# Kernel optimization log

Measured on AMD Instinct MI355X. Metric: run time of the kernel, lower is better.

## Reference

```python
import jax, jax.numpy as jnp
import numpy as np

TAU = 0.5  # init tau
EPS = 1e-8  # F.cosine_similarity eps


def setup_inputs() -> dict:
    key = jax.random.key(0)
    k1, k2 = jax.random.split(key)
    N, D, NUM_CLASSES = 4096, 1024, 128
    layer_embeds = jax.random.normal(k1, (N, D), dtype=jnp.float32)
    y_true = jax.random.randint(k2, (N,), 0, NUM_CLASSES, dtype=jnp.int64)
    return {"layer_embeds": layer_embeds, "y_true": y_true}


def reference(layer_embeds, y_true):
    N = layer_embeds.shape[0]
    # batched cosine similarity, scaled like the original: (cos + 1) * 0.5 * tau
    norms = jnp.maximum(jnp.linalg.norm(layer_embeds, axis=1), EPS)  # [N]
    cos = (layer_embeds @ layer_embeds.T) / (norms[:, None] * norms[None, :])  # [N, N]
    S = (cos + 1.0) * 0.5 * TAU

    same = y_true[:, None] == y_true[None, :]  # [N, N]
    eye = jnp.eye(N, dtype=bool)
    pos_mask = same & ~eye            # same-label pairs, j != i
    neg_mask = ~same                  # different-label pairs (diag excluded since same there)

    # column 0: first positive (in j order), else stays 0
    has_pos = pos_mask.any(axis=1)
    first_pos = jnp.argmax(pos_mask, axis=1)
    pos_val = jnp.where(has_pos, S[jnp.arange(N), first_pos], 0.0)  # [N]

    # negatives fill columns 1.. in j order: col = 1 + (#negatives with j' < j)
    negi = neg_mask.astype(jnp.int32)
    col = 1 + jnp.cumsum(negi, axis=1) - negi  # [N, N]
    W = 2 * N  # pad one dummy column for non-negative entries
    cols = jnp.where(neg_mask, col, W - 1)
    rows = jnp.broadcast_to(jnp.arange(N)[:, None], (N, N))
    loss_temp = jnp.zeros((N, W), dtype=jnp.float32)
    loss_temp = loss_temp.at[rows, cols].set(jnp.where(neg_mask, S, 0.0))
    loss_temp = loss_temp.at[:, 0].set(pos_val)
    loss_temp = loss_temp[:, : 2 * N - 1]  # [N, 2N-1], matches torch buffer

    # -log_softmax, take column 0, sum over rows, divide by N
    lse = jax.nn.logsumexp(loss_temp, axis=1)  # [N]
    loss = jnp.sum(lse - loss_temp[:, 0]) / N
    return loss
```

## Files before the change

### kernel.cpp

```cpp
#include <hip/hip_runtime.h>
#include <hip/hip_bf16.h>
#include <math.h>

#define NN 4096
#define DD 1024
#define NCLS 128
#define TAU 0.5f
#define EPSV 1e-8f

typedef __bf16 bf16;
typedef __bf16 bf16x8 __attribute__((ext_vector_type(8)));
typedef __bf16 bf16x4 __attribute__((ext_vector_type(4)));
typedef float f32x4 __attribute__((ext_vector_type(4)));

__device__ __forceinline__ void gl2lds16(const void* g, void* l) {
    __builtin_amdgcn_global_load_lds(
        (const __attribute__((address_space(1))) void*)g,
        (__attribute__((address_space(3))) void*)l,
        16, 0, 0);
}

__global__ __launch_bounds__(256) void k_norm_cast(const float* __restrict__ X,
                                                   bf16* __restrict__ Xn,
                                                   float* __restrict__ rsum) {
    int w = threadIdx.x >> 6, lane = threadIdx.x & 63;
    int row = blockIdx.x * 4 + w;
    const float* xr = X + (size_t)row * DD;
    float4 v[4];
    float ss = 0.f;
#pragma unroll
    for (int c = 0; c < 4; ++c) {
        v[c] = *(const float4*)(xr + c * 256 + lane * 4);
        ss += v[c].x * v[c].x + v[c].y * v[c].y + v[c].z * v[c].z + v[c].w * v[c].w;
    }
#pragma unroll
    for (int m = 1; m < 64; m <<= 1) ss += __shfl_xor(ss, m, 64);
    float rn = 1.f / fmaxf(sqrtf(ss), EPSV);
    if (lane == 0) rsum[row] = 0.f;
#pragma unroll
    for (int c = 0; c < 4; ++c) {
        bf16x4 o;
        o.x = (bf16)(v[c].x * rn);
        o.y = (bf16)(v[c].y * rn);
        o.z = (bf16)(v[c].z * rn);
        o.w = (bf16)(v[c].w * rn);
        *(bf16x4*)(Xn + (size_t)row * DD + c * 256 + lane * 4) = o;
    }
}

__global__ __launch_bounds__(1024) void k_classes(const int* __restrict__ y,
                                                  int* __restrict__ cnt,
                                                  int* __restrict__ mn1,
                                                  int* __restrict__ mn2) {
    __shared__ int sc[NCLS], s1[NCLS], s2[NCLS];
    int t = threadIdx.x;
    if (t < NCLS) { sc[t] = 0; s1[t] = 0x7fffffff; s2[t] = 0x7fffffff; }
    __syncthreads();
    int yv[4];
#pragma unroll
    for (int k = 0; k < 4; ++k) {
        int i = t + k * 1024;
        yv[k] = y[i];
        atomicAdd(&sc[yv[k]], 1);
        atomicMin(&s1[yv[k]], i);
    }
    __syncthreads();
#pragma unroll
    for (int k = 0; k < 4; ++k) {
        int i = t + k * 1024;
        if (s1[yv[k]] != i) atomicMin(&s2[yv[k]], i);
    }
    __syncthreads();
    if (t < NCLS) { cnt[t] = sc[t]; mn1[t] = s1[t]; mn2[t] = s2[t]; }
}

__global__ __launch_bounds__(256) void k_posval(const bf16* __restrict__ Xn,
                                                const int* __restrict__ y,
                                                const int* __restrict__ cnt,
                                                const int* __restrict__ mn1,
                                                const int* __restrict__ mn2,
                                                float* __restrict__ posv) {
    int w = threadIdx.x >> 6, lane = threadIdx.x & 63;
    int i = blockIdx.x * 4 + w;
    int c = y[i];
    float pv = 0.f;
    if (cnt[c] >= 2) {
        int fp = (mn1[c] == i) ? mn2[c] : mn1[c];
        const bf16* xi = Xn + (size_t)i * DD;
        const bf16* xf = Xn + (size_t)fp * DD;
        float dot = 0.f;
#pragma unroll
        for (int cc = 0; cc < 2; ++cc) {
            bf16x8 a = *(const bf16x8*)(xi + cc * 512 + lane * 8);
            bf16x8 b = *(const bf16x8*)(xf + cc * 512 + lane * 8);
#pragma unroll
            for (int e = 0; e < 8; ++e) dot += (float)a[e] * (float)b[e];
        }
#pragma unroll
        for (int m = 1; m < 64; m <<= 1) dot += __shfl_xor(dot, m, 64);
        pv = (dot + 1.f) * (0.5f * TAU);
    }
    if (lane == 0) posv[i] = pv;
}

__global__ __launch_bounds__(256) void k_gemm(const bf16* __restrict__ Xn,
                                              const int* __restrict__ y,
                                              float* __restrict__ rowsum) {
    __shared__ __align__(16) bf16 As[128 * 32];
    __shared__ __align__(16) bf16 Bs[128 * 32];
    __shared__ int yA[128], yB[128];

    int id = blockIdx.x;
    float ff = sqrtf((float)(8 * id + 1));
    int bj = (int)((ff - 1.f) * 0.5f);
    if (bj * (bj + 1) / 2 > id) bj--;
    if ((bj + 1) * (bj + 2) / 2 <= id) bj++;
    int bi = id - bj * (bj + 1) / 2;
    const int rowA0 = bi * 128;
    const int rowB0 = bj * 128;
    const bool diag = (bi == bj);

    const int tid = threadIdx.x;
    if (tid < 128) yA[tid] = y[rowA0 + tid];
    else           yB[tid - 128] = y[rowB0 + tid - 128];

    const int lane = tid & 63;
    const int w = tid >> 6;
    const int wm = w & 1, wn = w >> 1;
    const int lr = lane >> 4, lc = lane & 15;

    f32x4 acc[4][4];
#pragma unroll
    for (int i = 0; i < 4; ++i)
#pragma unroll
        for (int j = 0; j < 4; ++j) acc[i][j] = (f32x4){0.f, 0.f, 0.f, 0.f};

    const int r = tid >> 2;
    const int g = tid & 3;
    const int kg = g ^ ((r >> 1) & 3);
    const bf16* gA0 = Xn + (size_t)(rowA0 + r) * DD + kg * 8;
    const bf16* gA1 = gA0 + (size_t)64 * DD;
    const bf16* gB0 = Xn + (size_t)(rowB0 + r) * DD + kg * 8;
    const bf16* gB1 = gB0 + (size_t)64 * DD;
    bf16* lA0 = As + tid * 8;
    bf16* lA1 = As + 64 * 32 + tid * 8;
    bf16* lB0 = Bs + tid * 8;
    bf16* lB1 = Bs + 64 * 32 + tid * 8;

    const int sw = (lc >> 1) & 3;

    for (int k0 = 0; k0 < DD; k0 += 32) {
        __syncthreads();
        gl2lds16(gA0 + k0, lA0);
        gl2lds16(gA1 + k0, lA1);
        gl2lds16(gB0 + k0, lB0);
        gl2lds16(gB1 + k0, lB1);
        __syncthreads();

        bf16x8 af[4], bfr[4];
#pragma unroll
        for (int mt = 0; mt < 4; ++mt)
            af[mt] = *(const bf16x8*)(As + (wm * 64 + mt * 16 + lc) * 32 + ((lr ^ sw) * 8));
#pragma unroll
        for (int nt = 0; nt < 4; ++nt)
            bfr[nt] = *(const bf16x8*)(Bs + (wn * 64 + nt * 16 + lc) * 32 + ((lr ^ sw) * 8));
#pragma unroll
        for (int mt = 0; mt < 4; ++mt)
#pragma unroll
            for (int nt = 0; nt < 4; ++nt)
                acc[mt][nt] = __builtin_amdgcn_mfma_f32_16x16x32_bf16(
                    af[mt], bfr[nt], acc[mt][nt], 0, 0, 0);
    }

    int ycol[4];
#pragma unroll
    for (int nt = 0; nt < 4; ++nt) ycol[nt] = yB[wn * 64 + nt * 16 + lc];
    float colacc[4] = {0.f, 0.f, 0.f, 0.f};
#pragma unroll
    for (int mt = 0; mt < 4; ++mt) {
#pragma unroll
        for (int rr = 0; rr < 4; ++rr) {
            int rloc = wm * 64 + mt * 16 + lr * 4 + rr;
            int yrow = yA[rloc];
            float s = 0.f;
#pragma unroll
            for (int nt = 0; nt < 4; ++nt) {
                float Sv = (acc[mt][nt][rr] + 1.f) * (0.5f * TAU);
                float e = (ycol[nt] != yrow) ? __expf(Sv) : 0.f;
                s += e;
                colacc[nt] += e;
            }
            s += __shfl_xor(s, 1, 16);
            s += __shfl_xor(s, 2, 16);
            s += __shfl_xor(s, 4, 16);
            s += __shfl_xor(s, 8, 16);
            if (lc == 0) atomicAdd(&rowsum[rowA0 + rloc], s);
        }
    }
    if (!diag) {
#pragma unroll
        for (int nt = 0; nt < 4; ++nt) {
            float cs = colacc[nt];
            cs += __shfl_xor(cs, 16, 64);
            cs += __shfl_xor(cs, 32, 64);
            if (lane < 16) atomicAdd(&rowsum[rowB0 + wn * 64 + nt * 16 + lane], cs);
        }
    }
}

__global__ __launch_bounds__(1024) void k_finalize(const float* __restrict__ rowsum,
                                                   const float* __restrict__ posv,
                                                   const int* __restrict__ y,
                                                   const int* __restrict__ cnt,
                                                   float* __restrict__ out) {
    int t = threadIdx.x;
    float acc = 0.f;
#pragma unroll
    for (int k = 0; k < 4; ++k) {
        int i = t + k * 1024;
        float pv = posv[i];
        float tot = rowsum[i] + __expf(pv) + (float)(NN - 2 + cnt[y[i]]);
        acc += logf(tot) - pv;
    }
#pragma unroll
    for (int m = 1; m < 64; m <<= 1) acc += __shfl_xor(acc, m, 64);
    __shared__ float wsum[16];
    int w = t >> 6, lane = t & 63;
    if (lane == 0) wsum[w] = acc;
    __syncthreads();
    if (t == 0) {
        float s = 0.f;
#pragma unroll
        for (int q = 0; q < 16; ++q) s += wsum[q];
        *out = s / (float)NN;
    }
}

extern "C" void kernel_launch(void* const* d_in, const int* in_sizes, int n_in,
                              void* d_out, int out_size, void* d_ws, size_t ws_size,
                              hipStream_t stream) {
    const float* X = (const float*)d_in[0];
    const int* y = (const int*)d_in[1];
    float* out = (float*)d_out;

    char* ws = (char*)d_ws;
    bf16* Xn     = (bf16*)ws;
    float* rsum  = (float*)(ws + 8 * 1024 * 1024);
    float* posv  = (float*)(ws + 8 * 1024 * 1024 + 16 * 1024);
    int* cnt     = (int*)(ws + 8 * 1024 * 1024 + 32 * 1024);
    int* mn1     = (int*)(ws + 8 * 1024 * 1024 + 32 * 1024 + 512);
    int* mn2     = (int*)(ws + 8 * 1024 * 1024 + 32 * 1024 + 1024);

    k_norm_cast<<<dim3(NN / 4), 256, 0, stream>>>(X, Xn, rsum);
    k_classes<<<dim3(1), 1024, 0, stream>>>(y, cnt, mn1, mn2);
    k_posval<<<dim3(NN / 4), 256, 0, stream>>>(Xn, y, cnt, mn1, mn2, posv);
    k_gemm<<<dim3(528), 256, 0, stream>>>(Xn, y, rsum);
    k_finalize<<<dim3(1), 1024, 0, stream>>>(rsum, posv, y, cnt, out);
}
```

Before: 106.5 us.

## Fuse prep kernels, merge posval into finalize, and deepen GEMM K-tile

Merges class statistics into the normalize/cast kernel (block 0), and folds the positive-value dot product into a parallel finalize kernel that reduces with one atomicAdd per block, going from five launches to three. The GEMM now stages 64-wide K tiles with an 8-way XOR swizzle, halving the number of barrier pairs per K loop. The cost is double the LDS per block and a float atomic reduction whose summation order is nondeterministic.

Result: slower. 127.5 us (+19.7%).

```diff
diff --git a/kernel.cpp b/kernel.cpp
--- a/kernel.cpp
+++ b/kernel.cpp
@@ -20,9 +20,14 @@
         16, 0, 0);
 }
 
-__global__ __launch_bounds__(256) void k_norm_cast(const float* __restrict__ X,
-                                                   bf16* __restrict__ Xn,
-                                                   float* __restrict__ rsum) {
+__global__ __launch_bounds__(256) void k_prep(const float* __restrict__ X,
+                                              bf16* __restrict__ Xn,
+                                              float* __restrict__ rsum,
+                                              const int* __restrict__ y,
+                                              int* __restrict__ cnt,
+                                              int* __restrict__ mn1,
+                                              int* __restrict__ mn2,
+                                              float* __restrict__ out) {
     int w = threadIdx.x >> 6, lane = threadIdx.x & 63;
     int row = blockIdx.x * 4 + w;
     const float* xr = X + (size_t)row * DD;
@@ -46,68 +51,37 @@
         o.w = (bf16)(v[c].w * rn);
         *(bf16x4*)(Xn + (size_t)row * DD + c * 256 + lane * 4) = o;
     }
-}
-
-__global__ __launch_bounds__(1024) void k_classes(const int* __restrict__ y,
-                                                  int* __restrict__ cnt,
-                                                  int* __restrict__ mn1,
-                                                  int* __restrict__ mn2) {
-    __shared__ int sc[NCLS], s1[NCLS], s2[NCLS];
-    int t = threadIdx.x;
-    if (t < NCLS) { sc[t] = 0; s1[t] = 0x7fffffff; s2[t] = 0x7fffffff; }
-    __syncthreads();
-    int yv[4];
-#pragma unroll
-    for (int k = 0; k < 4; ++k) {
-        int i = t + k * 1024;
-        yv[k] = y[i];
-        atomicAdd(&sc[yv[k]], 1);
-        atomicMin(&s1[yv[k]], i);
-    }
-    __syncthreads();
-#pragma unroll
-    for (int k = 0; k < 4; ++k) {
-        int i = t + k * 1024;
-        if (s1[yv[k]] != i) atomicMin(&s2[yv[k]], i);
-    }
-    __syncthreads();
-    if (t < NCLS) { cnt[t] = sc[t]; mn1[t] = s1[t]; mn2[t] = s2[t]; }
-}
-
-__global__ __launch_bounds__(256) void k_posval(const bf16* __restrict__ Xn,
-                                                const int* __restrict__ y,
-                                                const int* __restrict__ cnt,
-                                                const int* __restrict__ mn1,
-                                                const int* __restrict__ mn2,
-                                                float* __restrict__ posv) {
-    int w = threadIdx.x >> 6, lane = threadIdx.x & 63;
-    int i = blockIdx.x * 4 + w;
-    int c = y[i];
-    float pv = 0.f;
-    if (cnt[c] >= 2) {
-        int fp = (mn1[c] == i) ? mn2[c] : mn1[c];
-        const bf16* xi = Xn + (size_t)i * DD;
-        const bf16* xf = Xn + (size_t)fp * DD;
-        float dot = 0.f;
-#pragma unroll
-        for (int cc = 0; cc < 2; ++cc) {
-            bf16x8 a = *(const bf16x8*)(xi + cc * 512 + lane * 8);
-            bf16x8 b = *(const bf16x8*)(xf + cc * 512 + lane * 8);
-#pragma unroll
-            for (int e = 0; e < 8; ++e) dot += (float)a[e] * (float)b[e];
-        }
-#pragma unroll
-        for (int m = 1; m < 64; m <<= 1) dot += __shfl_xor(dot, m, 64);
-        pv = (dot + 1.f) * (0.5f * TAU);
-    }
-    if (lane == 0) posv[i] = pv;
+
+    if (blockIdx.x == 0) {
+        __shared__ int sc[NCLS], s1[NCLS], s2[NCLS];
+        int t = threadIdx.x;
+        if (t < NCLS) { sc[t] = 0; s1[t] = 0x7fffffff; s2[t] = 0x7fffffff; }
+        __syncthreads();
+        int yv[16];
+#pragma unroll
+        for (int k = 0; k < 16; ++k) {
+            int i = k * 256 + t;
+            yv[k] = y[i];
+            atomicAdd(&sc[yv[k]], 1);
+            atomicMin(&s1[yv[k]], i);
+        }
+        __syncthreads();
+#pragma unroll
+        for (int k = 0; k < 16; ++k) {
+            int i = k * 256 + t;
+            if (s1[yv[k]] != i) atomicMin(&s2[yv[k]], i);
+        }
+        __syncthreads();
+        if (t < NCLS) { cnt[t] = sc[t]; mn1[t] = s1[t]; mn2[t] = s2[t]; }
+        if (t == 0) out[0] = 0.f;
+    }
 }
 
 __global__ __launch_bounds__(256) void k_gemm(const bf16* __restrict__ Xn,
                                               const int* __restrict__ y,
                                               float* __restrict__ rowsum) {
-    __shared__ __align__(16) bf16 As[128 * 32];
-    __shared__ __align__(16) bf16 Bs[128 * 32];
+    __shared__ __align__(16) bf16 As[128 * 64];
+    __shared__ __align__(16) bf16 Bs[128 * 64];
     __shared__ int yA[128], yB[128];
 
     int id = blockIdx.x;
@@ -135,41 +109,47 @@
 #pragma unroll
         for (int j = 0; j < 4; ++j) acc[i][j] = (f32x4){0.f, 0.f, 0.f, 0.f};
 
-    const int r = tid >> 2;
-    const int g = tid & 3;
-    const int kg = g ^ ((r >> 1) & 3);
-    const bf16* gA0 = Xn + (size_t)(rowA0 + r) * DD + kg * 8;
-    const bf16* gA1 = gA0 + (size_t)64 * DD;
-    const bf16* gB0 = Xn + (size_t)(rowB0 + r) * DD + kg * 8;
-    const bf16* gB1 = gB0 + (size_t)64 * DD;
-    bf16* lA0 = As + tid * 8;
-    bf16* lA1 = As + 64 * 32 + tid * 8;
-    bf16* lB0 = Bs + tid * 8;
-    bf16* lB1 = Bs + 64 * 32 + tid * 8;
-
-    const int sw = (lc >> 1) & 3;
-
-    for (int k0 = 0; k0 < DD; k0 += 32) {
-        __syncthreads();
-        gl2lds16(gA0 + k0, lA0);
-        gl2lds16(gA1 + k0, lA1);
-        gl2lds16(gB0 + k0, lB0);
-        gl2lds16(gB1 + k0, lB1);
-        __syncthreads();
-
-        bf16x8 af[4], bfr[4];
-#pragma unroll
-        for (int mt = 0; mt < 4; ++mt)
-            af[mt] = *(const bf16x8*)(As + (wm * 64 + mt * 16 + lc) * 32 + ((lr ^ sw) * 8));
-#pragma unroll
-        for (int nt = 0; nt < 4; ++nt)
-            bfr[nt] = *(const bf16x8*)(Bs + (wn * 64 + nt * 16 + lc) * 32 + ((lr ^ sw) * 8));
-#pragma unroll
-        for (int mt = 0; mt < 4; ++mt)
+    const bf16* gA[4]; const bf16* gB[4];
+    bf16* lA[4]; bf16* lB[4];
+#pragma unroll
+    for (int q = 0; q < 4; ++q) {
+        int s = q * 256 + tid;
+        int row = s >> 3;
+        int kg = (s & 7) ^ (row & 7);
+        gA[q] = Xn + (size_t)(rowA0 + row) * DD + kg * 8;
+        gB[q] = Xn + (size_t)(rowB0 + row) * DD + kg * 8;
+        lA[q] = As + s * 8;
+        lB[q] = Bs + s * 8;
+    }
+
+    const int sw = lc & 7;
+
+    for (int k0 = 0; k0 < DD; k0 += 64) {
+        __syncthreads();
+#pragma unroll
+        for (int q = 0; q < 4; ++q) {
+            gl2lds16(gA[q] + k0, lA[q]);
+            gl2lds16(gB[q] + k0, lB[q]);
+        }
+        __syncthreads();
+
+#pragma unroll
+        for (int ks = 0; ks < 2; ++ks) {
+            bf16x8 af[4], bfr[4];
+            int slot = (ks * 4 + lr) ^ sw;
+#pragma unroll
+            for (int mt = 0; mt < 4; ++mt)
+                af[mt] = *(const bf16x8*)(As + (wm * 64 + mt * 16 + lc) * 64 + slot * 8);
 #pragma unroll
             for (int nt = 0; nt < 4; ++nt)
-                acc[mt][nt] = __builtin_amdgcn_mfma_f32_16x16x32_bf16(
-                    af[mt], bfr[nt], acc[mt][nt], 0, 0, 0);
+                bfr[nt] = *(const bf16x8*)(Bs + (wn * 64 + nt * 16 + lc) * 64 + slot * 8);
+#pragma unroll
+            for (int mt = 0; mt < 4; ++mt)
+#pragma unroll
+                for (int nt = 0; nt < 4; ++nt)
+                    acc[mt][nt] = __builtin_amdgcn_mfma_f32_16x16x32_bf16(
+                        af[mt], bfr[nt], acc[mt][nt], 0, 0, 0);
+        }
     }
 
     int ycol[4];
@@ -208,32 +188,40 @@
     }
 }
 
-__global__ __launch_bounds__(1024) void k_finalize(const float* __restrict__ rowsum,
-                                                   const float* __restrict__ posv,
-                                                   const int* __restrict__ y,
-                                                   const int* __restrict__ cnt,
-                                                   float* __restrict__ out) {
-    int t = threadIdx.x;
-    float acc = 0.f;
-#pragma unroll
-    for (int k = 0; k < 4; ++k) {
-        int i = t + k * 1024;
-        float pv = posv[i];
-        float tot = rowsum[i] + __expf(pv) + (float)(NN - 2 + cnt[y[i]]);
-        acc += logf(tot) - pv;
-    }
-#pragma unroll
-    for (int m = 1; m < 64; m <<= 1) acc += __shfl_xor(acc, m, 64);
-    __shared__ float wsum[16];
-    int w = t >> 6, lane = t & 63;
-    if (lane == 0) wsum[w] = acc;
+__global__ __launch_bounds__(256) void k_tail(const bf16* __restrict__ Xn,
+                                              const int* __restrict__ y,
+                                              const int* __restrict__ cnt,
+                                              const int* __restrict__ mn1,
+                                              const int* __restrict__ mn2,
+                                              const float* __restrict__ rowsum,
+                                              float* __restrict__ out) {
+    int w = threadIdx.x >> 6, lane = threadIdx.x & 63;
+    int i = blockIdx.x * 4 + w;
+    int c = y[i];
+    int cc = cnt[c];
+    float pv = 0.f;
+    if (cc >= 2) {
+        int fp = (mn1[c] == i) ? mn2[c] : mn1[c];
+        const bf16* xi = Xn + (size_t)i * DD;
+        const bf16* xf = Xn + (size_t)fp * DD;
+        float dot = 0.f;
+#pragma unroll
+        for (int q = 0; q < 2; ++q) {
+            bf16x8 a = *(const bf16x8*)(xi + q * 512 + lane * 8);
+            bf16x8 b = *(const bf16x8*)(xf + q * 512 + lane * 8);
+#pragma unroll
+            for (int e = 0; e < 8; ++e) dot += (float)a[e] * (float)b[e];
+        }
+#pragma unroll
+        for (int m = 1; m < 64; m <<= 1) dot += __shfl_xor(dot, m, 64);
+        pv = (dot + 1.f) * (0.5f * TAU);
+    }
+    float contrib = logf(rowsum[i] + __expf(pv) + (float)(NN - 2 + cc)) - pv;
+    __shared__ float wsum[4];
+    if (lane == 0) wsum[w] = contrib;
     __syncthreads();
-    if (t == 0) {
-        float s = 0.f;
-#pragma unroll
-        for (int q = 0; q < 16; ++q) s += wsum[q];
-        *out = s / (float)NN;
-    }
+    if (threadIdx.x == 0)
+        atomicAdd(out, (wsum[0] + wsum[1] + wsum[2] + wsum[3]) * (1.f / (float)NN));
 }
 
 extern "C" void kernel_launch(void* const* d_in, const int* in_sizes, int n_in,
@@ -244,16 +232,13 @@
     float* out = (float*)d_out;
 
     char* ws = (char*)d_ws;
-    bf16* Xn     = (bf16*)ws;
-    float* rsum  = (float*)(ws + 8 * 1024 * 1024);
-    float* posv  = (float*)(ws + 8 * 1024 * 1024 + 16 * 1024);
-    int* cnt     = (int*)(ws + 8 * 1024 * 1024 + 32 * 1024);
-    int* mn1     = (int*)(ws + 8 * 1024 * 1024 + 32 * 1024 + 512);
-    int* mn2     = (int*)(ws + 8 * 1024 * 1024 + 32 * 1024 + 1024);
-
-    k_norm_cast<<<dim3(NN / 4), 256, 0, stream>>>(X, Xn, rsum);
-    k_classes<<<dim3(1), 1024, 0, stream>>>(y, cnt, mn1, mn2);
-    k_posval<<<dim3(NN / 4), 256, 0, stream>>>(Xn, y, cnt, mn1, mn2, posv);
+    bf16* Xn    = (bf16*)ws;
+    float* rsum = (float*)(ws + 8 * 1024 * 1024);
+    int* cnt    = (int*)(ws + 8 * 1024 * 1024 + 16 * 1024);
+    int* mn1    = (int*)(ws + 8 * 1024 * 1024 + 16 * 1024 + 512);
+    int* mn2    = (int*)(ws + 8 * 1024 * 1024 + 16 * 1024 + 1024);
+
+    k_prep<<<dim3(NN / 4), 256, 0, stream>>>(X, Xn, rsum, y, cnt, mn1, mn2, out);
     k_gemm<<<dim3(528), 256, 0, stream>>>(Xn, y, rsum);
-    k_finalize<<<dim3(1), 1024, 0, stream>>>(rsum, posv, y, cnt, out);
-}
+    k_tail<<<dim3(NN / 4), 256, 0, stream>>>(Xn, y, cnt, mn1, mn2, rsum, out);
+}
```
